# Kernel optimization log

Hardware: AMD Instinct MI355X
Metric: run time of the kernel (lower is better)

Reference implementation:

```python
import jax, jax.numpy as jnp
import numpy as np

D_IN = 784
D = 768          # hidden_dim
R = 8            # num_rels
L = 3            # num_layers
B = 64           # graphs in batch
N = 32768        # total nodes
E = 262144       # total edges


def _layer_norm(x, g, b, eps=1e-5):
    m = x.mean(-1, keepdims=True)
    v = x.var(-1, keepdims=True)
    return (x - m) / jnp.sqrt(v + eps) * g + b


def setup_inputs() -> dict:
    key = jax.random.key(0)
    ks = jax.random.split(key, 24)
    s = 0.02
    inp = {
        "type_vec": jax.random.normal(ks[0], (N, 16), jnp.float32),
        "code_vec": jax.random.normal(ks[1], (N, D), jnp.float32),
        # input_proj: Linear(784,768) + LayerNorm(768)
        "W_in": jax.random.normal(ks[2], (D_IN, D), jnp.float32) * s,
        "b_in": jnp.zeros((D,), jnp.float32),
        "ln_in_g": jnp.ones((D,), jnp.float32),
        "ln_in_b": jnp.zeros((D,), jnp.float32),
        # RGCN layers (basis regularizer, num_bases=num_rels -> per-relation W)
        "W_rel": jax.random.normal(ks[3], (L, R, D, D), jnp.float32) * s,
        "W_loop": jax.random.normal(ks[4], (L, D, D), jnp.float32) * s,
        "rgcn_bias": jnp.zeros((L, D), jnp.float32),
        "ln_g": jnp.ones((L, D), jnp.float32),
        "ln_b": jnp.zeros((L, D), jnp.float32),
        # global attention pooling gate MLP: 768 -> 384 -> 1
        "Wg1": jax.random.normal(ks[5], (D, D // 2), jnp.float32) * s,
        "bg1": jnp.zeros((D // 2,), jnp.float32),
        "Wg2": jax.random.normal(ks[6], (D // 2, 1), jnp.float32) * s,
        "bg2": jnp.zeros((1,), jnp.float32),
        # classifier: 768 -> 512 (+LN) -> 2
        "Wc1": jax.random.normal(ks[7], (D, 512), jnp.float32) * s,
        "bc1": jnp.zeros((512,), jnp.float32),
        "ln_c_g": jnp.ones((512,), jnp.float32),
        "ln_c_b": jnp.zeros((512,), jnp.float32),
        "Wc2": jax.random.normal(ks[8], (512, 2), jnp.float32) * s,
        "bc2": jnp.zeros((2,), jnp.float32),
        # graph structure
        "src": jax.random.randint(ks[9], (E,), 0, N, jnp.int64),
        "dst": jax.random.randint(ks[10], (E,), 0, N, jnp.int64),
        "edge_type": jax.random.randint(ks[11], (E,), 0, R, jnp.int64),
        "node_graph": jnp.sort(jax.random.randint(ks[12], (N,), 0, B, jnp.int64)),
        "num_graphs": B,
    }
    return inp


def reference(type_vec, code_vec, W_in, b_in, ln_in_g, ln_in_b,
              W_rel, W_loop, rgcn_bias, ln_g, ln_b,
              Wg1, bg1, Wg2, bg2, Wc1, bc1, ln_c_g, ln_c_b, Wc2, bc2,
              src, dst, edge_type, node_graph, num_graphs):
    # input projection
    h = jnp.concatenate([type_vec, code_vec], axis=-1)           # [N, 784]
    h = jax.nn.gelu(_layer_norm(h @ W_in + b_in, ln_in_g, ln_in_b), approximate=False)
    n_nodes = h.shape[0]
    n_layers, n_rels = W_rel.shape[0], W_rel.shape[1]

    for l in range(n_layers):
        agg = jnp.zeros_like(h)
        for r in range(n_rels):
            # relation-specific transform, then gather->mask->scatter-add
            msg = (h @ W_rel[l, r])[src] * (edge_type == r).astype(h.dtype)[:, None]  # [E, D]
            agg = agg + jax.ops.segment_sum(msg, dst, num_segments=n_nodes)
        h_new = agg + rgcn_bias[l] + h @ W_loop[l]               # DGL: agg + bias + self-loop
        h = jax.nn.gelu(_layer_norm(h_new, ln_g[l], ln_b[l]), approximate=False)

    # global attention pooling (segment softmax over nodes of each graph)
    gate = (jax.nn.gelu(h @ Wg1 + bg1, approximate=False) @ Wg2 + bg2)[:, 0]  # [N]
    gmax = jax.ops.segment_max(gate, node_graph, num_segments=num_graphs)
    e = jnp.exp(gate - gmax[node_graph])
    denom = jax.ops.segment_sum(e, node_graph, num_segments=num_graphs)
    w = e / denom[node_graph]
    graph_repr = jax.ops.segment_sum(w[:, None] * h, node_graph, num_segments=num_graphs)  # [B, D]

    # classifier head
    z = jax.nn.gelu(_layer_norm(graph_repr @ Wc1 + bc1, ln_c_g, ln_c_b), approximate=False)
    logits = z @ Wc2 + bc2
    return jax.nn.log_softmax(logits, axis=-1)
```

## Files before the change

### kernel.cpp

```cpp
#include <hip/hip_runtime.h>
#include <hip/hip_bf16.h>

typedef __hip_bfloat16 bf16;
typedef __attribute__((ext_vector_type(8))) __bf16 bf16x8;
typedef __attribute__((ext_vector_type(4))) float f32x4;

#define N_NODES 32768
#define N_EDGES 262144
#define DIM 768
#define NGR 64
#define KIN 800
#define KSTACK 6912

#define GLOBAL_AS __attribute__((address_space(1)))
#define LDS_AS __attribute__((address_space(3)))

__device__ __forceinline__ float gelu_f(float x) {
    return 0.5f * x * (1.0f + erff(x * 0.70710678118654752f));
}
__device__ __forceinline__ float bfu(unsigned short v) {
    union { unsigned u; float f; } x; x.u = (unsigned)v << 16; return x.f;
}
__device__ __forceinline__ unsigned short fbf(float f) {
    bf16 t = __float2bfloat16(f); return *(unsigned short*)&t;
}

__global__ __launch_bounds__(256)
void tcast_k(const float* __restrict__ in, bf16* __restrict__ out, int I, int O,
             int Ipad, int ostride) {
    __shared__ float t[32][33];
    const int i0 = blockIdx.x * 32, o0 = blockIdx.y * 32;
    const int tx = threadIdx.x & 31, ty = threadIdx.x >> 5;
#pragma unroll
    for (int q = 0; q < 4; ++q) {
        int i = i0 + ty + q * 8, o = o0 + tx;
        t[ty + q * 8][tx] = (i < I) ? in[(size_t)i * O + o] : 0.0f;
    }
    __syncthreads();
#pragma unroll
    for (int q = 0; q < 4; ++q) {
        int o = o0 + ty + q * 8, i = i0 + tx;
        if (i < Ipad) out[(size_t)o * ostride + i] = __float2bfloat16(t[tx][ty + q * 8]);
    }
}

__global__ __launch_bounds__(256)
void wprep_k(const float* __restrict__ W_rel, const float* __restrict__ W_loop,
             bf16* __restrict__ Wst) {
    __shared__ float t[32][33];
    const int z = blockIdx.z, l = z / 9, q = z % 9;
    const float* in = (q < 8) ? W_rel + ((size_t)(l * 8 + q)) * DIM * DIM
                              : W_loop + (size_t)l * DIM * DIM;
    bf16* out = Wst + (size_t)l * DIM * KSTACK + (q < 8 ? (q + 1) * DIM : 0);
    const int i0 = blockIdx.x * 32, o0 = blockIdx.y * 32;
    const int tx = threadIdx.x & 31, ty = threadIdx.x >> 5;
#pragma unroll
    for (int qq = 0; qq < 4; ++qq)
        t[ty + qq * 8][tx] = in[(size_t)(i0 + ty + qq * 8) * DIM + o0 + tx];
    __syncthreads();
#pragma unroll
    for (int qq = 0; qq < 4; ++qq)
        out[(size_t)(o0 + ty + qq * 8) * KSTACK + i0 + tx] =
            __float2bfloat16(t[tx][ty + qq * 8]);
}

__global__ __launch_bounds__(256)
void concat_k(const float* __restrict__ tv, const float* __restrict__ cv, bf16* __restrict__ X) {
    const int n = blockIdx.x;
    for (int c = threadIdx.x; c < KIN; c += 256) {
        float v = 0.0f;
        if (c < 16) v = tv[(size_t)n * 16 + c];
        else if (c < 784) v = cv[(size_t)n * DIM + (c - 16)];
        X[(size_t)n * KIN + c] = __float2bfloat16(v);
    }
}

__global__ __launch_bounds__(256)
void hist_k(const int* __restrict__ dst, int* __restrict__ deg) {
    int e = blockIdx.x * 256 + threadIdx.x;
    if (e < N_EDGES) atomicAdd(&deg[dst[e]], 1);
}

__global__ __launch_bounds__(1024)
void scan_k(const int* __restrict__ deg, int* __restrict__ row_ptr, int* __restrict__ cursor) {
    __shared__ int part[1024];
    const int t = threadIdx.x;
    int loc[32]; int s = 0;
#pragma unroll
    for (int i = 0; i < 32; ++i) { loc[i] = s; s += deg[t * 32 + i]; }
    part[t] = s; __syncthreads();
    for (int st = 1; st < 1024; st <<= 1) {
        int v = (t >= st) ? part[t - st] : 0;
        __syncthreads();
        part[t] += v;
        __syncthreads();
    }
    const int base = part[t] - s;
#pragma unroll
    for (int i = 0; i < 32; ++i) { int v = base + loc[i]; row_ptr[t * 32 + i] = v; cursor[t * 32 + i] = v; }
    if (t == 1023) row_ptr[N_NODES] = part[1023];
}

__global__ __launch_bounds__(256)
void place_k(const int* __restrict__ src, const int* __restrict__ dst,
             const int* __restrict__ et, int* __restrict__ cursor, int* __restrict__ eidx) {
    int e = blockIdx.x * 256 + threadIdx.x;
    if (e >= N_EDGES) return;
    int d = dst[e];
    int pos = atomicAdd(&cursor[d], 1);
    eidx[pos] = (src[e] & 0xffff) | (et[e] << 16);
}

template <int NC>
__global__ __launch_bounds__(256)
void gather_k(const bf16* __restrict__ h, const int* __restrict__ row_ptr,
              const int* __restrict__ eidx, bf16* __restrict__ AGG, int rbase) {
    const int wave = threadIdx.x >> 6, lane = threadIdx.x & 63;
    const int n = blockIdx.x * 4 + wave;
    const int start = row_ptr[n], end = row_ptr[n + 1];
    const int c0 = 2 * lane;
    float2 f0[6] = {}, f1[6] = {}, f2[6] = {}, f3[6] = {};
#define ACCJ(F) _Pragma("unroll") for (int j = 0; j < 6; ++j) { F[j].x += bfu(u[j].x); F[j].y += bfu(u[j].y); }
    for (int e = start; e < end; ++e) {
        const int pk = eidx[e];
        const int sel = (pk >> 16) - rbase;
        if (sel < 0 || sel >= NC) continue;
        const unsigned short* hs = (const unsigned short*)&h[(size_t)(pk & 0xffff) * DIM];
        ushort2 u[6];
#pragma unroll
        for (int j = 0; j < 6; ++j) u[j] = *(const ushort2*)&hs[c0 + j * 128];
        if (sel == 0) { ACCJ(f0) }
        else if (NC > 1 && sel == 1) { ACCJ(f1) }
        else if (NC > 2 && sel == 2) { ACCJ(f2) }
        else if (NC > 3 && sel == 3) { ACCJ(f3) }
    }
#undef ACCJ
    unsigned short* outrow = (unsigned short*)&AGG[(size_t)n * (NC * DIM)];
#define STJ(F, S) _Pragma("unroll") for (int j = 0; j < 6; ++j) { ushort2 o; o.x = fbf(F[j].x); o.y = fbf(F[j].y); *(ushort2*)&outrow[(S) * DIM + c0 + j * 128] = o; }
    STJ(f0, 0)
    if (NC > 1) { STJ(f1, 1) }
    if (NC > 2) { STJ(f2, 2) }
    if (NC > 3) { STJ(f3, 3) }
#undef STJ
}

template <int ACCUM>
__global__ __launch_bounds__(256, 2)
void gemm_bt(const bf16* __restrict__ A1, int S1, int K1,
             const bf16* __restrict__ A2, int S2,
             const bf16* __restrict__ BT, int ldb,
             float* __restrict__ OUT, int Nn, int Ktot) {
    __shared__ __align__(16) unsigned short lA[128 * 32];
    __shared__ __align__(16) unsigned short lB[128 * 32];
    const int bn = blockIdx.x * 128;
    const int bm = blockIdx.y * 128;
    const int tid = threadIdx.x;
    const int wave = tid >> 6, lane = tid & 63;
    const int wr = wave >> 1, wc = wave & 1;
    const int l15 = lane & 15, lg = lane >> 4;

    f32x4 acc[4][4] = {};

    for (int k0 = 0; k0 < Ktot; k0 += 32) {
        const bf16* Ab; int koff, stA;
        if (k0 < K1) { Ab = A1; koff = k0; stA = S1; }
        else         { Ab = A2; koff = k0 - K1; stA = S2; }
#pragma unroll
        for (int q = 0; q < 2; ++q) {
            int c = wave * 128 + q * 64 + lane;
            int row = c >> 2, k8 = c & 3;
            const bf16* ga = Ab + (size_t)(bm + row) * stA + koff + k8 * 8;
            const bf16* gb = BT + (size_t)(bn + row) * ldb + k0 + k8 * 8;
            __builtin_amdgcn_global_load_lds((const GLOBAL_AS void*)ga,
                (LDS_AS void*)&lA[(wave * 128 + q * 64) * 8], 16, 0, 0);
            __builtin_amdgcn_global_load_lds((const GLOBAL_AS void*)gb,
                (LDS_AS void*)&lB[(wave * 128 + q * 64) * 8], 16, 0, 0);
        }
        __syncthreads();
        bf16x8 af[4], bfr[4];
#pragma unroll
        for (int mi = 0; mi < 4; ++mi)
            af[mi] = *reinterpret_cast<const bf16x8*>(&lA[(wr * 64 + mi * 16 + l15) * 32 + lg * 8]);
#pragma unroll
        for (int ni = 0; ni < 4; ++ni)
            bfr[ni] = *reinterpret_cast<const bf16x8*>(&lB[(wc * 64 + ni * 16 + l15) * 32 + lg * 8]);
#pragma unroll
        for (int mi = 0; mi < 4; ++mi)
#pragma unroll
            for (int ni = 0; ni < 4; ++ni)
                acc[mi][ni] = __builtin_amdgcn_mfma_f32_16x16x32_bf16(af[mi], bfr[ni], acc[mi][ni], 0, 0, 0);
        __syncthreads();
    }

#pragma unroll
    for (int mi = 0; mi < 4; ++mi)
#pragma unroll
        for (int ni = 0; ni < 4; ++ni) {
            const int r0 = bm + wr * 64 + mi * 16 + lg * 4;
            const int c0 = bn + wc * 64 + ni * 16 + l15;
#pragma unroll
            for (int i = 0; i < 4; ++i) {
                size_t idx = (size_t)(r0 + i) * Nn + c0;
                float v = acc[mi][ni][i];
                if (ACCUM) v += OUT[idx];
                OUT[idx] = v;
            }
        }
}

__global__ __launch_bounds__(256)
void ln_gelu_k(const float* __restrict__ ACC, const float* __restrict__ bias,
               const float* __restrict__ g, const float* __restrict__ b,
               bf16* __restrict__ hout) {
    const int wave = threadIdx.x >> 6, lane = threadIdx.x & 63;
    const int n = blockIdx.x * 4 + wave;
    float x[12];
    float s = 0.f, ss = 0.f;
#pragma unroll
    for (int j = 0; j < 12; ++j) {
        int c = lane + j * 64;
        x[j] = ACC[(size_t)n * DIM + c] + bias[c];
        s += x[j]; ss += x[j] * x[j];
    }
#pragma unroll
    for (int m = 1; m < 64; m <<= 1) { s += __shfl_xor(s, m, 64); ss += __shfl_xor(ss, m, 64); }
    const float mean = s * (1.f / DIM);
    const float var = ss * (1.f / DIM) - mean * mean;
    const float rstd = rsqrtf(var + 1e-5f);
#pragma unroll
    for (int j = 0; j < 12; ++j) {
        int c = lane + j * 64;
        float y = (x[j] - mean) * rstd * g[c] + b[c];
        hout[(size_t)n * DIM + c] = __float2bfloat16(gelu_f(y));
    }
}

__global__ __launch_bounds__(256)
void gate_k(const float* __restrict__ G1, const float* __restrict__ bg1,
            const float* __restrict__ Wg2, const float* __restrict__ bg2,
            float* __restrict__ gate) {
    const int wave = threadIdx.x >> 6, lane = threadIdx.x & 63;
    const int n = blockIdx.x * 4 + wave;
    float acc = 0.f;
#pragma unroll
    for (int j = 0; j < 6; ++j) {
        int c = lane + j * 64;
        float xv = G1[(size_t)n * 384 + c] + bg1[c];
        acc += gelu_f(xv) * Wg2[c];
    }
#pragma unroll
    for (int m = 1; m < 64; m <<= 1) acc += __shfl_xor(acc, m, 64);
    if (lane == 0) gate[n] = acc + bg2[0];
}

__device__ __forceinline__ int lower_bound_ng(const int* ng, int key) {
    int lo = 0, hi = N_NODES;
    while (lo < hi) { int mid = (lo + hi) >> 1; if (ng[mid] < key) lo = mid + 1; else hi = mid; }
    return lo;
}

__global__ __launch_bounds__(256)
void seg_stats_k(const float* __restrict__ gate, const int* __restrict__ ng,
                 float* __restrict__ gmax, float* __restrict__ gden) {
    __shared__ float red[256];
    const int b = blockIdx.x, t = threadIdx.x;
    const int start = lower_bound_ng(ng, b), end = lower_bound_ng(ng, b + 1);
    float m = -1e30f;
    for (int n = start + t; n < end; n += 256) m = fmaxf(m, gate[n]);
    red[t] = m; __syncthreads();
    for (int s = 128; s > 0; s >>= 1) { if (t < s) red[t] = fmaxf(red[t], red[t + s]); __syncthreads(); }
    const float gm = red[0]; __syncthreads();
    float ssum = 0.f;
    for (int n = start + t; n < end; n += 256) ssum += expf(gate[n] - gm);
    red[t] = ssum; __syncthreads();
    for (int s = 128; s > 0; s >>= 1) { if (t < s) red[t] += red[t + s]; __syncthreads(); }
    if (t == 0) { gmax[b] = gm; gden[b] = fmaxf(red[0], 1e-30f); }
}

__global__ __launch_bounds__(768)
void pool_k(const bf16* __restrict__ h, const float* __restrict__ gate,
            const int* __restrict__ ng, const float* __restrict__ gmax,
            const float* __restrict__ gden, float* __restrict__ grep) {
    const int b = blockIdx.x, c = threadIdx.x;
    const int start = lower_bound_ng(ng, b), end = lower_bound_ng(ng, b + 1);
    const float gm = gmax[b], inv = 1.0f / gden[b];
    const unsigned short* hv = (const unsigned short*)h;
    float a0 = 0.f, a1 = 0.f;
    int n = start;
    for (; n + 1 < end; n += 2) {
        float w0 = expf(gate[n] - gm) * inv;
        float w1 = expf(gate[n + 1] - gm) * inv;
        a0 += w0 * bfu(hv[(size_t)n * DIM + c]);
        a1 += w1 * bfu(hv[(size_t)(n + 1) * DIM + c]);
    }
    if (n < end) a0 += expf(gate[n] - gm) * inv * bfu(hv[(size_t)n * DIM + c]);
    grep[(size_t)b * DIM + c] = a0 + a1;
}

__global__ __launch_bounds__(512)
void cls_k(const float* __restrict__ grep, const float* __restrict__ Wc1,
           const float* __restrict__ bc1, const float* __restrict__ lng,
           const float* __restrict__ lnb, const float* __restrict__ Wc2,
           const float* __restrict__ bc2, float* __restrict__ out) {
    __shared__ float gr[DIM];
    __shared__ float red[512];
    const int b = blockIdx.x, j = threadIdx.x;
    for (int c = j; c < DIM; c += 512) gr[c] = grep[(size_t)b * DIM + c];
    __syncthreads();
    float a = bc1[j];
#pragma unroll 4
    for (int k = 0; k < DIM; ++k) a = fmaf(gr[k], Wc1[(size_t)k * 512 + j], a);
    red[j] = a; __syncthreads();
    for (int s = 256; s > 0; s >>= 1) { if (j < s) red[j] += red[j + s]; __syncthreads(); }
    const float mean = red[0] * (1.f / 512.f);
    __syncthreads();
    red[j] = (a - mean) * (a - mean); __syncthreads();
    for (int s = 256; s > 0; s >>= 1) { if (j < s) red[j] += red[j + s]; __syncthreads(); }
    const float rstd = rsqrtf(red[0] * (1.f / 512.f) + 1e-5f);
    __syncthreads();
    const float z = gelu_f((a - mean) * rstd * lng[j] + lnb[j]);
    red[j] = z * Wc2[2 * j + 0]; __syncthreads();
    for (int s = 256; s > 0; s >>= 1) { if (j < s) red[j] += red[j + s]; __syncthreads(); }
    const float l0 = red[0] + bc2[0];
    __syncthreads();
    red[j] = z * Wc2[2 * j + 1]; __syncthreads();
    for (int s = 256; s > 0; s >>= 1) { if (j < s) red[j] += red[j + s]; __syncthreads(); }
    if (j == 0) {
        const float l1 = red[0] + bc2[1];
        const float mx = fmaxf(l0, l1);
        const float lse = mx + logf(expf(l0 - mx) + expf(l1 - mx));
        out[2 * b + 0] = l0 - lse;
        out[2 * b + 1] = l1 - lse;
    }
}

extern "C" void kernel_launch(void* const* d_in, const int* in_sizes, int n_in,
                              void* d_out, int out_size, void* d_ws, size_t ws_size,
                              hipStream_t stream) {
    const float* type_vec = (const float*)d_in[0];
    const float* code_vec = (const float*)d_in[1];
    const float* W_in     = (const float*)d_in[2];
    const float* b_in     = (const float*)d_in[3];
    const float* ln_in_g  = (const float*)d_in[4];
    const float* ln_in_b  = (const float*)d_in[5];
    const float* W_rel    = (const float*)d_in[6];
    const float* W_loop   = (const float*)d_in[7];
    const float* rgcn_bias= (const float*)d_in[8];
    const float* ln_g     = (const float*)d_in[9];
    const float* ln_b     = (const float*)d_in[10];
    const float* Wg1      = (const float*)d_in[11];
    const float* bg1      = (const float*)d_in[12];
    const float* Wg2      = (const float*)d_in[13];
    const float* bg2      = (const float*)d_in[14];
    const float* Wc1      = (const float*)d_in[15];
    const float* bc1      = (const float*)d_in[16];
    const float* ln_c_g   = (const float*)d_in[17];
    const float* ln_c_b   = (const float*)d_in[18];
    const float* Wc2      = (const float*)d_in[19];
    const float* bc2      = (const float*)d_in[20];
    const int* src        = (const int*)d_in[21];
    const int* dst        = (const int*)d_in[22];
    const int* etype      = (const int*)d_in[23];
    const int* node_graph = (const int*)d_in[24];

    char* ws = (char*)d_ws;

    auto need = [](int nc) -> size_t {
        size_t base = 0;
        auto al = [&](size_t sz) { size_t r = base; base = (base + sz + 255) & ~(size_t)255; (void)r; };
        al((size_t)N_NODES * DIM * 2);
        al((size_t)N_NODES * DIM * 4);
        al((size_t)DIM * KIN * 2);
        al((size_t)3 * DIM * KSTACK * 2);
        al((size_t)384 * DIM * 2);
        size_t open = base;
        al((size_t)N_NODES * nc * DIM * 2);
        al((size_t)(N_NODES + 1) * 4);
        al((size_t)N_NODES * 4);
        al((size_t)N_NODES * 4);
        al((size_t)N_EDGES * 4);
        al((size_t)N_NODES * 4);
        al(256); al(256);
        al((size_t)NGR * DIM * 4);
        size_t xend = open + (size_t)N_NODES * KIN * 2;
        return base > xend ? base : xend;
    };
    int nc = 1;
    if (ws_size >= need(4)) nc = 4;
    else if (ws_size >= need(2)) nc = 2;

    size_t off = 0;
    auto alloc = [&](size_t sz) { size_t r = off; off = (off + sz + 255) & ~(size_t)255; return r; };
    bf16*  h_bf  = (bf16*)(ws + alloc((size_t)N_NODES * DIM * 2));
    float* ACC   = (float*)(ws + alloc((size_t)N_NODES * DIM * 4));
    bf16*  WinT  = (bf16*)(ws + alloc((size_t)DIM * KIN * 2));
    bf16*  Wst   = (bf16*)(ws + alloc((size_t)3 * DIM * KSTACK * 2));
    bf16*  Wg1T  = (bf16*)(ws + alloc((size_t)384 * DIM * 2));
    size_t open  = off;
    bf16*  AGG   = (bf16*)(ws + alloc((size_t)N_NODES * nc * DIM * 2));
    int*   row_ptr = (int*)(ws + alloc((size_t)(N_NODES + 1) * 4));
    int*   cursor  = (int*)(ws + alloc((size_t)N_NODES * 4));
    int*   deg     = (int*)(ws + alloc((size_t)N_NODES * 4));
    int*   eidx    = (int*)(ws + alloc((size_t)N_EDGES * 4));
    float* gate  = (float*)(ws + alloc((size_t)N_NODES * 4));
    float* gmax  = (float*)(ws + alloc(256));
    float* gden  = (float*)(ws + alloc(256));
    float* grep  = (float*)(ws + alloc((size_t)NGR * DIM * 4));
    bf16*  Xbf   = (bf16*)(ws + open);
    float* G1    = ACC;

    tcast_k<<<dim3(25, 24), 256, 0, stream>>>(W_in, WinT, 784, DIM, KIN, KIN);
    wprep_k<<<dim3(24, 24, 27), 256, 0, stream>>>(W_rel, W_loop, Wst);
    tcast_k<<<dim3(24, 12), 256, 0, stream>>>(Wg1, Wg1T, DIM, 384, DIM, DIM);

    concat_k<<<N_NODES, 256, 0, stream>>>(type_vec, code_vec, Xbf);
    gemm_bt<0><<<dim3(DIM / 128, N_NODES / 128), 256, 0, stream>>>(
        Xbf, KIN, KIN, Xbf, KIN, WinT, KIN, ACC, DIM, KIN);
    ln_gelu_k<<<N_NODES / 4, 256, 0, stream>>>(ACC, b_in, ln_in_g, ln_in_b, h_bf);

    hipMemsetAsync(deg, 0, (size_t)N_NODES * 4, stream);
    hist_k<<<N_EDGES / 256, 256, 0, stream>>>(dst, deg);
    scan_k<<<1, 1024, 0, stream>>>(deg, row_ptr, cursor);
    place_k<<<N_EDGES / 256, 256, 0, stream>>>(src, dst, etype, cursor, eidx);

    const int nchunks = 8 / nc;
    for (int l = 0; l < 3; ++l) {
        bf16* Wl = Wst + (size_t)l * DIM * KSTACK;
        for (int c = 0; c < nchunks; ++c) {
            const int rbase = c * nc;
            if (nc == 1)      gather_k<1><<<N_NODES / 4, 256, 0, stream>>>(h_bf, row_ptr, eidx, AGG, rbase);
            else if (nc == 2) gather_k<2><<<N_NODES / 4, 256, 0, stream>>>(h_bf, row_ptr, eidx, AGG, rbase);
            else              gather_k<4><<<N_NODES / 4, 256, 0, stream>>>(h_bf, row_ptr, eidx, AGG, rbase);
            if (c == 0) {
                gemm_bt<0><<<dim3(DIM / 128, N_NODES / 128), 256, 0, stream>>>(
                    h_bf, DIM, DIM, AGG, nc * DIM, Wl, KSTACK, ACC, DIM, DIM + nc * DIM);
            } else {
                gemm_bt<1><<<dim3(DIM / 128, N_NODES / 128), 256, 0, stream>>>(
                    AGG, nc * DIM, nc * DIM, AGG, nc * DIM,
                    Wl + DIM + c * nc * DIM, KSTACK, ACC, DIM, nc * DIM);
            }
        }
        ln_gelu_k<<<N_NODES / 4, 256, 0, stream>>>(ACC, rgcn_bias + l * DIM, ln_g + l * DIM,
                                                   ln_b + l * DIM, h_bf);
    }

    gemm_bt<0><<<dim3(384 / 128, N_NODES / 128), 256, 0, stream>>>(
        h_bf, DIM, DIM, h_bf, DIM, Wg1T, DIM, G1, 384, DIM);
    gate_k<<<N_NODES / 4, 256, 0, stream>>>(G1, bg1, Wg2, bg2, gate);
    seg_stats_k<<<NGR, 256, 0, stream>>>(gate, node_graph, gmax, gden);
    pool_k<<<NGR, 768, 0, stream>>>(h_bf, gate, node_graph, gmax, gden, grep);

    cls_k<<<NGR, 512, 0, stream>>>(grep, Wc1, bc1, ln_c_g, ln_c_b, Wc2, bc2, (float*)d_out);
}
```

Before: 2.751 ms.

## Bucket edges by (dst, relation) and use 128x256 GEMM tiles with XCD swizzle

The edge CSR is now keyed by destination node and relation type, so each gather chunk reads only the edges of its own relations. It no longer scans and filters every incoming edge, and the per-edge record no longer packs the relation. The input projection and RGCN GEMMs move to a new 512-thread kernel with a 128x256 output tile and a block-id swizzle across the 8 XCDs, aimed at better B-tile reuse and L2 locality. The cost is an 8x larger histogram, scan and cursor array built by a single-block scan doing 256 serial elements per thread. Larger tiles also mean fewer workgroups per CU and a bigger LDS footprint.

New measurement: 2.774 ms. About the same (+0.9%).

```diff
diff --git a/kernel.cpp b/kernel.cpp
--- a/kernel.cpp
+++ b/kernel.cpp
@@ -11,6 +11,7 @@
 #define NGR 64
 #define KIN 800
 #define KSTACK 6912
+#define NKEY (N_NODES * 8)
 
 #define GLOBAL_AS __attribute__((address_space(1)))
 #define LDS_AS __attribute__((address_space(3)))
@@ -76,18 +77,18 @@
 }
 
 __global__ __launch_bounds__(256)
-void hist_k(const int* __restrict__ dst, int* __restrict__ deg) {
+void hist2_k(const int* __restrict__ dst, const int* __restrict__ et, int* __restrict__ deg) {
     int e = blockIdx.x * 256 + threadIdx.x;
-    if (e < N_EDGES) atomicAdd(&deg[dst[e]], 1);
+    if (e < N_EDGES) atomicAdd(&deg[dst[e] * 8 + et[e]], 1);
 }
 
 __global__ __launch_bounds__(1024)
-void scan_k(const int* __restrict__ deg, int* __restrict__ row_ptr, int* __restrict__ cursor) {
+void scan2_k(const int* __restrict__ deg, int* __restrict__ rp, int* __restrict__ cur) {
     __shared__ int part[1024];
     const int t = threadIdx.x;
-    int loc[32]; int s = 0;
-#pragma unroll
-    for (int i = 0; i < 32; ++i) { loc[i] = s; s += deg[t * 32 + i]; }
+    const int base_i = t * 256;
+    int s = 0;
+    for (int i = 0; i < 256; ++i) s += deg[base_i + i];
     part[t] = s; __syncthreads();
     for (int st = 1; st < 1024; st <<= 1) {
         int v = (t >= st) ? part[t - st] : 0;
@@ -95,53 +96,122 @@
         part[t] += v;
         __syncthreads();
     }
-    const int base = part[t] - s;
-#pragma unroll
-    for (int i = 0; i < 32; ++i) { int v = base + loc[i]; row_ptr[t * 32 + i] = v; cursor[t * 32 + i] = v; }
-    if (t == 1023) row_ptr[N_NODES] = part[1023];
-}
-
-__global__ __launch_bounds__(256)
-void place_k(const int* __restrict__ src, const int* __restrict__ dst,
-             const int* __restrict__ et, int* __restrict__ cursor, int* __restrict__ eidx) {
+    int run = part[t] - s;
+    for (int i = 0; i < 256; ++i) {
+        int d = deg[base_i + i];
+        rp[base_i + i] = run; cur[base_i + i] = run;
+        run += d;
+    }
+    if (t == 1023) rp[NKEY] = run;
+}
+
+__global__ __launch_bounds__(256)
+void place2_k(const int* __restrict__ src, const int* __restrict__ dst,
+              const int* __restrict__ et, int* __restrict__ cur, int* __restrict__ eidx) {
     int e = blockIdx.x * 256 + threadIdx.x;
     if (e >= N_EDGES) return;
-    int d = dst[e];
-    int pos = atomicAdd(&cursor[d], 1);
-    eidx[pos] = (src[e] & 0xffff) | (et[e] << 16);
+    int pos = atomicAdd(&cur[dst[e] * 8 + et[e]], 1);
+    eidx[pos] = src[e];
 }
 
 template <int NC>
 __global__ __launch_bounds__(256)
-void gather_k(const bf16* __restrict__ h, const int* __restrict__ row_ptr,
-              const int* __restrict__ eidx, bf16* __restrict__ AGG, int rbase) {
+void gather2_k(const bf16* __restrict__ h, const int* __restrict__ rp2,
+               const int* __restrict__ eidx, bf16* __restrict__ AGG, int rbase) {
     const int wave = threadIdx.x >> 6, lane = threadIdx.x & 63;
     const int n = blockIdx.x * 4 + wave;
-    const int start = row_ptr[n], end = row_ptr[n + 1];
     const int c0 = 2 * lane;
-    float2 f0[6] = {}, f1[6] = {}, f2[6] = {}, f3[6] = {};
-#define ACCJ(F) _Pragma("unroll") for (int j = 0; j < 6; ++j) { F[j].x += bfu(u[j].x); F[j].y += bfu(u[j].y); }
-    for (int e = start; e < end; ++e) {
-        const int pk = eidx[e];
-        const int sel = (pk >> 16) - rbase;
-        if (sel < 0 || sel >= NC) continue;
-        const unsigned short* hs = (const unsigned short*)&h[(size_t)(pk & 0xffff) * DIM];
-        ushort2 u[6];
-#pragma unroll
-        for (int j = 0; j < 6; ++j) u[j] = *(const ushort2*)&hs[c0 + j * 128];
-        if (sel == 0) { ACCJ(f0) }
-        else if (NC > 1 && sel == 1) { ACCJ(f1) }
-        else if (NC > 2 && sel == 2) { ACCJ(f2) }
-        else if (NC > 3 && sel == 3) { ACCJ(f3) }
-    }
-#undef ACCJ
     unsigned short* outrow = (unsigned short*)&AGG[(size_t)n * (NC * DIM)];
-#define STJ(F, S) _Pragma("unroll") for (int j = 0; j < 6; ++j) { ushort2 o; o.x = fbf(F[j].x); o.y = fbf(F[j].y); *(ushort2*)&outrow[(S) * DIM + c0 + j * 128] = o; }
-    STJ(f0, 0)
-    if (NC > 1) { STJ(f1, 1) }
-    if (NC > 2) { STJ(f2, 2) }
-    if (NC > 3) { STJ(f3, 3) }
-#undef STJ
+    const int* bp = &rp2[n * 8 + rbase];
+#pragma unroll 1
+    for (int sel = 0; sel < NC; ++sel) {
+        const int s = bp[sel], e = bp[sel + 1];
+        float2 f[6] = {};
+        for (int t = s; t < e; ++t) {
+            const unsigned short* hs = (const unsigned short*)&h[(size_t)eidx[t] * DIM];
+#pragma unroll
+            for (int j = 0; j < 6; ++j) {
+                ushort2 u = *(const ushort2*)&hs[c0 + j * 128];
+                f[j].x += bfu(u.x); f[j].y += bfu(u.y);
+            }
+        }
+#pragma unroll
+        for (int j = 0; j < 6; ++j) {
+            ushort2 o; o.x = fbf(f[j].x); o.y = fbf(f[j].y);
+            *(ushort2*)&outrow[sel * DIM + c0 + j * 128] = o;
+        }
+    }
+}
+
+template <int ACCUM>
+__global__ __launch_bounds__(512, 2)
+void gemm256(const bf16* __restrict__ A1, int S1, int K1,
+             const bf16* __restrict__ A2, int S2,
+             const bf16* __restrict__ BT, int ldb,
+             float* __restrict__ OUT, int Nn, int Ktot, int nbx) {
+    __shared__ __align__(16) unsigned short lA[128 * 32];
+    __shared__ __align__(16) unsigned short lB[256 * 32];
+    const int nblk = gridDim.x;
+    const int qx = nblk >> 3;
+    const int bid = blockIdx.x;
+    const int wgid = (bid & 7) * qx + (bid >> 3);
+    const int bx = wgid % nbx, by = wgid / nbx;
+    const int bn = bx * 256, bm = by * 128;
+    const int tid = threadIdx.x;
+    const int wave = tid >> 6, lane = tid & 63;
+    const int wr = wave >> 2, wc = wave & 3;
+    const int l15 = lane & 15, lg = lane >> 4;
+
+    f32x4 acc[4][4] = {};
+
+    for (int k0 = 0; k0 < Ktot; k0 += 32) {
+        const bf16* Ab; int koff, stA;
+        if (k0 < K1) { Ab = A1; koff = k0; stA = S1; }
+        else         { Ab = A2; koff = k0 - K1; stA = S2; }
+        {
+            const int row = tid >> 2, k8 = tid & 3;
+            const bf16* ga = Ab + (size_t)(bm + row) * stA + koff + k8 * 8;
+            __builtin_amdgcn_global_load_lds((const GLOBAL_AS void*)ga,
+                (LDS_AS void*)&lA[(wave * 64) * 8], 16, 0, 0);
+        }
+#pragma unroll
+        for (int qq = 0; qq < 2; ++qq) {
+            const int c = qq * 512 + tid;
+            const int row = c >> 2, k8 = c & 3;
+            const bf16* gb = BT + (size_t)(bn + row) * ldb + k0 + k8 * 8;
+            __builtin_amdgcn_global_load_lds((const GLOBAL_AS void*)gb,
+                (LDS_AS void*)&lB[((qq * 8 + wave) * 64) * 8], 16, 0, 0);
+        }
+        __syncthreads();
+        bf16x8 af[4], bfr[4];
+#pragma unroll
+        for (int mi = 0; mi < 4; ++mi)
+            af[mi] = *reinterpret_cast<const bf16x8*>(&lA[(wr * 64 + mi * 16 + l15) * 32 + lg * 8]);
+#pragma unroll
+        for (int ni = 0; ni < 4; ++ni)
+            bfr[ni] = *reinterpret_cast<const bf16x8*>(&lB[(wc * 64 + ni * 16 + l15) * 32 + lg * 8]);
+#pragma unroll
+        for (int mi = 0; mi < 4; ++mi)
+#pragma unroll
+            for (int ni = 0; ni < 4; ++ni)
+                acc[mi][ni] = __builtin_amdgcn_mfma_f32_16x16x32_bf16(af[mi], bfr[ni], acc[mi][ni], 0, 0, 0);
+        __syncthreads();
+    }
+
+#pragma unroll
+    for (int mi = 0; mi < 4; ++mi)
+#pragma unroll
+        for (int ni = 0; ni < 4; ++ni) {
+            const int r0 = bm + wr * 64 + mi * 16 + lg * 4;
+            const int c0 = bn + wc * 64 + ni * 16 + l15;
+#pragma unroll
+            for (int i = 0; i < 4; ++i) {
+                size_t idx = (size_t)(r0 + i) * Nn + c0;
+                float v = acc[mi][ni][i];
+                if (ACCUM) v += OUT[idx];
+                OUT[idx] = v;
+            }
+        }
 }
 
 template <int ACCUM>
@@ -367,7 +437,7 @@
 
     auto need = [](int nc) -> size_t {
         size_t base = 0;
-        auto al = [&](size_t sz) { size_t r = base; base = (base + sz + 255) & ~(size_t)255; (void)r; };
+        auto al = [&](size_t sz) { base = (base + sz + 255) & ~(size_t)255; };
         al((size_t)N_NODES * DIM * 2);
         al((size_t)N_NODES * DIM * 4);
         al((size_t)DIM * KIN * 2);
@@ -375,9 +445,9 @@
         al((size_t)384 * DIM * 2);
         size_t open = base;
         al((size_t)N_NODES * nc * DIM * 2);
-        al((size_t)(N_NODES + 1) * 4);
-        al((size_t)N_NODES * 4);
-        al((size_t)N_NODES * 4);
+        al((size_t)(NKEY + 1) * 4);
+        al((size_t)NKEY * 4);
+        al((size_t)NKEY * 4);
         al((size_t)N_EDGES * 4);
         al((size_t)N_NODES * 4);
         al(256); al(256);
@@ -398,10 +468,10 @@
     bf16*  Wg1T  = (bf16*)(ws + alloc((size_t)384 * DIM * 2));
     size_t open  = off;
     bf16*  AGG   = (bf16*)(ws + alloc((size_t)N_NODES * nc * DIM * 2));
-    int*   row_ptr = (int*)(ws + alloc((size_t)(N_NODES + 1) * 4));
-    int*   cursor  = (int*)(ws + alloc((size_t)N_NODES * 4));
-    int*   deg     = (int*)(ws + alloc((size_t)N_NODES * 4));
-    int*   eidx    = (int*)(ws + alloc((size_t)N_EDGES * 4));
+    int*   rp2   = (int*)(ws + alloc((size_t)(NKEY + 1) * 4));
+    int*   cur2  = (int*)(ws + alloc((size_t)NKEY * 4));
+    int*   deg2  = (int*)(ws + alloc((size_t)NKEY * 4));
+    int*   eidx  = (int*)(ws + alloc((size_t)N_EDGES * 4));
     float* gate  = (float*)(ws + alloc((size_t)N_NODES * 4));
     float* gmax  = (float*)(ws + alloc(256));
     float* gden  = (float*)(ws + alloc(256));
@@ -414,37 +484,36 @@
     tcast_k<<<dim3(24, 12), 256, 0, stream>>>(Wg1, Wg1T, DIM, 384, DIM, DIM);
 
     concat_k<<<N_NODES, 256, 0, stream>>>(type_vec, code_vec, Xbf);
-    gemm_bt<0><<<dim3(DIM / 128, N_NODES / 128), 256, 0, stream>>>(
-        Xbf, KIN, KIN, Xbf, KIN, WinT, KIN, ACC, DIM, KIN);
+    gemm256<0><<<768, 512, 0, stream>>>(Xbf, KIN, KIN, Xbf, KIN, WinT, KIN, ACC, DIM, KIN, 3);
     ln_gelu_k<<<N_NODES / 4, 256, 0, stream>>>(ACC, b_in, ln_in_g, ln_in_b, h_bf);
 
-    hipMemsetAsync(deg, 0, (size_t)N_NODES * 4, stream);
-    hist_k<<<N_EDGES / 256, 256, 0, stream>>>(dst, deg);
-    scan_k<<<1, 1024, 0, stream>>>(deg, row_ptr, cursor);
-    place_k<<<N_EDGES / 256, 256, 0, stream>>>(src, dst, etype, cursor, eidx);
+    hipMemsetAsync(deg2, 0, (size_t)NKEY * 4, stream);
+    hist2_k<<<N_EDGES / 256, 256, 0, stream>>>(dst, etype, deg2);
+    scan2_k<<<1, 1024, 0, stream>>>(deg2, rp2, cur2);
+    place2_k<<<N_EDGES / 256, 256, 0, stream>>>(src, dst, etype, cur2, eidx);
 
     const int nchunks = 8 / nc;
     for (int l = 0; l < 3; ++l) {
         bf16* Wl = Wst + (size_t)l * DIM * KSTACK;
         for (int c = 0; c < nchunks; ++c) {
             const int rbase = c * nc;
-            if (nc == 1)      gather_k<1><<<N_NODES / 4, 256, 0, stream>>>(h_bf, row_ptr, eidx, AGG, rbase);
-            else if (nc == 2) gather_k<2><<<N_NODES / 4, 256, 0, stream>>>(h_bf, row_ptr, eidx, AGG, rbase);
-            else              gather_k<4><<<N_NODES / 4, 256, 0, stream>>>(h_bf, row_ptr, eidx, AGG, rbase);
+            if (nc == 1)      gather2_k<1><<<N_NODES / 4, 256, 0, stream>>>(h_bf, rp2, eidx, AGG, rbase);
+            else if (nc == 2) gather2_k<2><<<N_NODES / 4, 256, 0, stream>>>(h_bf, rp2, eidx, AGG, rbase);
+            else              gather2_k<4><<<N_NODES / 4, 256, 0, stream>>>(h_bf, rp2, eidx, AGG, rbase);
             if (c == 0) {
-                gemm_bt<0><<<dim3(DIM / 128, N_NODES / 128), 256, 0, stream>>>(
-                    h_bf, DIM, DIM, AGG, nc * DIM, Wl, KSTACK, ACC, DIM, DIM + nc * DIM);
+                gemm256<0><<<768, 512, 0, stream>>>(
+                    h_bf, DIM, DIM, AGG, nc * DIM, Wl, KSTACK, ACC, DIM, DIM + nc * DIM, 3);
             } else {
-                gemm_bt<1><<<dim3(DIM / 128, N_NODES / 128), 256, 0, stream>>>(
+                gemm256<1><<<768, 512, 0, stream>>>(
                     AGG, nc * DIM, nc * DIM, AGG, nc * DIM,
-                    Wl + DIM + c * nc * DIM, KSTACK, ACC, DIM, nc * DIM);
+                    Wl + (size_t)DIM * (1 + rbase), KSTACK, ACC, DIM, nc * DIM, 3);
             }
         }
         ln_gelu_k<<<N_NODES / 4, 256, 0, stream>>>(ACC, rgcn_bias + l * DIM, ln_g + l * DIM,
                                                    ln_b + l * DIM, h_bf);
     }
 
-    gemm_bt<0><<<dim3(384 / 128, N_NODES / 128), 256, 0, stream>>>(
+    gemm_bt<0><<<dim3(3, 256), 256, 0, stream>>>(
         h_bf, DIM, DIM, h_bf, DIM, Wg1T, DIM, G1, 384, DIM);
     gate_k<<<N_NODES / 4, 256, 0, stream>>>(G1, bg1, Wg2, bg2, gate);
     seg_stats_k<<<NGR, 256, 0, stream>>>(gate, node_graph, gmax, gden);
```
